# Optimization experiments

Measured on AMD Instinct MI355X. Metric: run time of the kernel, lower is better.

The kernel has to match this reference:

```python
import jax, jax.numpy as jnp
import numpy as np

B, T, E = 2, 2048, 2048
H, D = 16, 128
KVH = H // 2
THETA = 10000.0

def make_rope(dim, seq_len, theta):
    inv_freqs = 1.0 / (theta ** (jnp.arange(0, dim, 2, dtype=jnp.float32) / dim))
    positions = jnp.arange(seq_len, dtype=jnp.float32)
    freqs = positions[:, None] * inv_freqs[None, :]  # (T, D/2)
    return jax.lax.complex(jnp.cos(freqs), jnp.sin(freqs))

def apply_rope(x, rope):
    # x: (B, h, T, D), rope: (T, D/2) complex
    xr = x.astype(jnp.float32).reshape(*x.shape[:-1], -1, 2)
    xc = jax.lax.complex(xr[..., 0], xr[..., 1])
    out = xc * rope[None, None, :, :]
    return jnp.stack([jnp.real(out), jnp.imag(out)], axis=-1).reshape(x.shape).astype(x.dtype)

def setup_inputs() -> dict:
    key = jax.random.key(0)
    ks = jax.random.split(key, 5)
    x = jax.random.normal(ks[0], (B, T, E), dtype=jnp.float32)
    mask = jnp.tril(jnp.ones((T, T), dtype=jnp.int32))[None, None]  # causal (1,1,T,T)
    s = 0.02
    wq = jax.random.normal(ks[1], (E, H * D), dtype=jnp.float32) * s
    wk = jax.random.normal(ks[2], (E, KVH * D), dtype=jnp.float32) * s
    wv = jax.random.normal(ks[3], (E, KVH * D), dtype=jnp.float32) * s
    wo = jax.random.normal(ks[4], (H * D, E), dtype=jnp.float32) * s
    return {"x": x, "mask": mask, "wq": wq, "wk": wk, "wv": wv, "wo": wo}

def reference(x, mask, wq, wk, wv, wo):
    rope = make_rope(D, T, THETA)
    q = (x @ wq).reshape(B, T, H, D).transpose(0, 2, 1, 3)      # (B,H,T,D)
    k = (x @ wk).reshape(B, T, KVH, D).transpose(0, 2, 1, 3)    # (B,KVH,T,D)
    v = (x @ wv).reshape(B, T, KVH, D).transpose(0, 2, 1, 3)
    q = apply_rope(q, rope)
    k = apply_rope(k, rope)
    # GQA: repeat kv heads to match query heads
    k = jnp.repeat(k, H // KVH, axis=1)
    v = jnp.repeat(v, H // KVH, axis=1)
    scale = D ** -0.5
    attn = jnp.einsum('bhqd,bhkd->bhqk', q, k) * scale
    attn = jnp.where(mask == 0, -jnp.inf, attn)
    attn = jax.nn.softmax(attn, axis=-1)
    attn = jnp.where(jnp.isnan(attn), 0.0, attn)
    out = jnp.einsum('bhqk,bhkd->bhqd', attn, v)
    out = out.transpose(0, 2, 1, 3).reshape(B, T, H * D)
    return out @ wo
```

## Files before the change

### kernel.cpp

```cpp
#include <hip/hip_runtime.h>
#include <math.h>

#define Bb   2
#define Tt   2048
#define Ee   2048
#define Hh   16
#define KVHh 8
#define Dd   128
#define Mm   (Bb*Tt)

typedef unsigned short u16;
typedef __bf16 bf16x8 __attribute__((ext_vector_type(8)));
typedef float  f32x4  __attribute__((ext_vector_type(4)));

__device__ __forceinline__ u16 f2b(float f) {
    union { float f; unsigned u; } v; v.f = f;
    unsigned r = v.u + 0x7fffu + ((v.u >> 16) & 1u);
    return (u16)(r >> 16);
}
__device__ __forceinline__ u16 f2b_fast(float f) {
    union { float f; unsigned u; } v; v.f = f;
    return (u16)((v.u + 0x8000u) >> 16);
}
__device__ __forceinline__ float b2f(u16 h) {
    union { float f; unsigned u; } v; v.u = ((unsigned)h) << 16;
    return v.f;
}

__device__ __forceinline__ void gl_lds16(const u16* g, u16* l) {
    __builtin_amdgcn_global_load_lds(
        (const __attribute__((address_space(1))) void*)g,
        (__attribute__((address_space(3))) void*)l,
        16, 0, 0);
}

__global__ void cast_x_kernel(const float* __restrict__ x, u16* __restrict__ xb, int n4) {
    int i = blockIdx.x * blockDim.x + threadIdx.x;
    if (i >= n4) return;
    float4 f = ((const float4*)x)[i];
    unsigned lo = (unsigned)f2b(f.x) | ((unsigned)f2b(f.y) << 16);
    unsigned hi = (unsigned)f2b(f.z) | ((unsigned)f2b(f.w) << 16);
    ((uint2*)xb)[i] = make_uint2(lo, hi);
}

__global__ void transpose_cast4_kernel(const float* __restrict__ wq, const float* __restrict__ wk,
                                       const float* __restrict__ wv, const float* __restrict__ wo,
                                       u16* __restrict__ btqkv, u16* __restrict__ bto) {
    __shared__ float tile[32][33];
    int job = blockIdx.z;
    const float* W; u16* Bt; int C;
    if (job == 0)      { W = wq; Bt = btqkv;                      C = 2048; }
    else if (job == 1) { W = wk; Bt = btqkv + (size_t)2048 * Ee;  C = 1024; }
    else if (job == 2) { W = wv; Bt = btqkv + (size_t)3072 * Ee;  C = 1024; }
    else               { W = wo; Bt = bto;                        C = 2048; }
    int c0 = blockIdx.x * 32, r0 = blockIdx.y * 32;
    if (c0 >= C) return;
    int x = threadIdx.x, y = threadIdx.y;
    for (int j = y; j < 32; j += 8)
        tile[j][x] = W[(size_t)(r0 + j) * C + c0 + x];
    __syncthreads();
    for (int j = y; j < 32; j += 8)
        Bt[(size_t)(c0 + j) * 2048 + r0 + x] = f2b(tile[x][j]);
}

__global__ void transpose_v_kernel(const u16* __restrict__ v, u16* __restrict__ vt) {
    __shared__ u16 tile[32][34];
    int x = threadIdx.x, y = threadIdx.y;
    int c0 = blockIdx.x * 32;
    int r0 = blockIdx.y * 32;
    int bk = blockIdx.z;
    for (int j = y; j < 32; j += 8)
        tile[j][x] = v[((size_t)bk * Tt + r0 + j) * Dd + c0 + x];
    __syncthreads();
    for (int j = y; j < 32; j += 8)
        vt[((size_t)bk * Dd + c0 + j) * Tt + r0 + x] = tile[x][j];
}

__global__ void rope_kernel(u16* __restrict__ q, u16* __restrict__ k) {
    const int QP = Bb * Hh * Tt * (Dd / 2);
    const int KP = Bb * KVHh * Tt * (Dd / 2);
    int idx = blockIdx.x * blockDim.x + threadIdx.x;
    if (idx >= QP + KP) return;
    u16* ptr; int p;
    if (idx < QP) { ptr = q; p = idx; } else { ptr = k; p = idx - QP; }
    int d2 = p & 63;
    int row = p >> 6;
    int t = row & (Tt - 1);
    float ex = (float)(2 * d2) * (1.0f / 128.0f);
    float inv = expf(-ex * 9.210340371976184f);
    float fr = (float)t * inv;
    float c = cosf(fr), s = sinf(fr);
    size_t e0 = (size_t)row * Dd + 2 * d2;
    unsigned pair = *(const unsigned*)(ptr + e0);
    float x0 = b2f((u16)(pair & 0xffff));
    float x1 = b2f((u16)(pair >> 16));
    float o0 = x0 * c - x1 * s;
    float o1 = x0 * s + x1 * c;
    *(unsigned*)(ptr + e0) = (unsigned)f2b(o0) | ((unsigned)f2b(o1) << 16);
}

__global__ __launch_bounds__(256) void gemm_kernel(
    const u16* __restrict__ A, const u16* __restrict__ Bt,
    int Mdim, int Ndim, int Kdim, int mode,
    u16* __restrict__ qo, u16* __restrict__ ko, u16* __restrict__ vo,
    float* __restrict__ fo)
{
    __shared__ u16 Ash[128 * 64];
    __shared__ u16 Bsh[128 * 64];
    int tid = threadIdx.x;
    int lane = tid & 63, wv = tid >> 6;
    int quad = lane >> 4, l15 = lane & 15;
    int bn = blockIdx.x, bm = blockIdx.y;
    int wm = (wv >> 1) * 64, wn = (wv & 1) * 64;
    const int rowA0 = bm * 128, rowB0 = bn * 128;
    int srow = lane >> 3;
    int scol = (lane & 7) * 8;

    f32x4 acc[4][4];
#pragma unroll
    for (int i = 0; i < 4; i++)
#pragma unroll
        for (int j = 0; j < 4; j++) acc[i][j] = (f32x4){0.f, 0.f, 0.f, 0.f};

    for (int kb = 0; kb < Kdim; kb += 64) {
#pragma unroll
        for (int j = 0; j < 4; j++) {
            int chunk = wv * 4 + j;
            int r = chunk * 8 + srow;
            gl_lds16(A  + (size_t)(rowA0 + r) * Kdim + kb + scol, Ash + chunk * 512);
            gl_lds16(Bt + (size_t)(rowB0 + r) * Kdim + kb + scol, Bsh + chunk * 512);
        }
        __syncthreads();
#pragma unroll
        for (int kc = 0; kc < 2; kc++) {
            bf16x8 af[4], bfr[4];
#pragma unroll
            for (int i = 0; i < 4; i++)
                af[i] = *(const bf16x8*)(Ash + (wm + i * 16 + l15) * 64 + kc * 32 + quad * 8);
#pragma unroll
            for (int i = 0; i < 4; i++)
                bfr[i] = *(const bf16x8*)(Bsh + (wn + i * 16 + l15) * 64 + kc * 32 + quad * 8);
#pragma unroll
            for (int i = 0; i < 4; i++)
#pragma unroll
                for (int j = 0; j < 4; j++)
                    acc[i][j] = __builtin_amdgcn_mfma_f32_16x16x32_bf16(af[i], bfr[j], acc[i][j], 0, 0, 0);
        }
        __syncthreads();
    }

#pragma unroll
    for (int i = 0; i < 4; i++)
#pragma unroll
        for (int j = 0; j < 4; j++)
#pragma unroll
            for (int r = 0; r < 4; r++) {
                int m = rowA0 + wm + i * 16 + quad * 4 + r;
                int n = rowB0 + wn + j * 16 + l15;
                float val = acc[i][j][r];
                if (mode == 0) {
                    int b = m >> 11, t = m & (Tt - 1);
                    if (n < 2048) {
                        int h = n >> 7, d = n & 127;
                        qo[(((size_t)(b * Hh + h)) * Tt + t) * Dd + d] = f2b(val);
                    } else if (n < 3072) {
                        int h = (n - 2048) >> 7, d = n & 127;
                        ko[(((size_t)(b * KVHh + h)) * Tt + t) * Dd + d] = f2b(val);
                    } else {
                        int h = (n - 3072) >> 7, d = n & 127;
                        vo[(((size_t)(b * KVHh + h)) * Tt + t) * Dd + d] = f2b(val);
                    }
                } else {
                    fo[(size_t)m * Ndim + n] = val;
                }
            }
}

#define LDKV 136
#define LDVT 72
#define LDP  72

__global__ __launch_bounds__(256) void flash_kernel(
    const u16* __restrict__ q, const u16* __restrict__ k, const u16* __restrict__ vt,
    u16* __restrict__ attn)
{
    __shared__ u16 Ksh[64 * LDKV];
    __shared__ u16 Vtsh[128 * LDVT];
    __shared__ u16 Psh[128 * LDP];

    int tid = threadIdx.x, lane = tid & 63, w = tid >> 6;
    int quad = lane >> 4, l15 = lane & 15;
    int pr = blockIdx.x;
    int bh = blockIdx.y;
    int b = bh >> 4, h = bh & 15;
    int kvh = h >> 1;
    const u16* qbase = q + (size_t)bh * Tt * Dd;
    const u16* kbase = k + ((size_t)(b * KVHh + kvh)) * Tt * Dd;
    const u16* vtbase = vt + ((size_t)(b * KVHh + kvh)) * Dd * Tt;
    u16* P0 = Psh + (2 * w) * 16 * LDP;
    u16* P1 = Psh + (2 * w + 1) * 16 * LDP;
    const float sc2 = 0.08838834764831845f * 1.4426950408889634f;

    for (int half = 0; half < 2; half++) {
        int qt = half ? (15 - pr) : pr;
        int row0 = qt * 128 + w * 32;

        bf16x8 qf0[4], qf1[4];
        {
            const u16* qr0 = qbase + (size_t)(row0 + l15) * Dd + quad * 8;
            const u16* qr1 = qbase + (size_t)(row0 + 16 + l15) * Dd + quad * 8;
#pragma unroll
            for (int c = 0; c < 4; c++) {
                qf0[c] = *(const bf16x8*)(qr0 + c * 32);
                qf1[c] = *(const bf16x8*)(qr1 + c * 32);
            }
        }

        f32x4 o0[8], o1[8];
#pragma unroll
        for (int i = 0; i < 8; i++) { o0[i] = (f32x4){0.f,0.f,0.f,0.f}; o1[i] = (f32x4){0.f,0.f,0.f,0.f}; }
        float l0[4] = {0.f,0.f,0.f,0.f}, l1[4] = {0.f,0.f,0.f,0.f};

        int nkt = 2 * (qt + 1);
        for (int kt = 0; kt < nkt; kt++) {
#pragma unroll
            for (int j = 0; j < 4; j++) {
                int chunk = j * 256 + tid;
                int rk = chunk >> 4, ck = chunk & 15;
                uint4 dk = *(const uint4*)(kbase + (size_t)(kt * 64 + rk) * Dd + ck * 8);
                *(uint4*)(Ksh + rk * LDKV + ck * 8) = dk;
                int rv = chunk >> 3, cv = chunk & 7;
                uint4 dv = *(const uint4*)(vtbase + (size_t)rv * Tt + kt * 64 + cv * 8);
                *(uint4*)(Vtsh + rv * LDVT + cv * 8) = dv;
            }
            __syncthreads();

            bool skip = (kt * 64) > (row0 + 31);
            if (!skip) {
                f32x4 s0[4], s1[4];
#pragma unroll
                for (int ni = 0; ni < 4; ni++) { s0[ni] = (f32x4){0.f,0.f,0.f,0.f}; s1[ni] = (f32x4){0.f,0.f,0.f,0.f}; }
#pragma unroll
                for (int c = 0; c < 4; c++)
#pragma unroll
                    for (int ni = 0; ni < 4; ni++) {
                        bf16x8 kf = *(const bf16x8*)(Ksh + (ni * 16 + l15) * LDKV + c * 32 + quad * 8);
                        s0[ni] = __builtin_amdgcn_mfma_f32_16x16x32_bf16(qf0[c], kf, s0[ni], 0, 0, 0);
                        s1[ni] = __builtin_amdgcn_mfma_f32_16x16x32_bf16(qf1[c], kf, s1[ni], 0, 0, 0);
                    }

                if (kt * 64 + 63 > row0) {
#pragma unroll
                    for (int ni = 0; ni < 4; ni++)
#pragma unroll
                        for (int r = 0; r < 4; r++) {
                            int kcol = kt * 64 + ni * 16 + l15;
                            int qa = row0 + quad * 4 + r;
                            int qb2 = row0 + 16 + quad * 4 + r;
                            if (kcol > qa)  s0[ni][r] = -__builtin_inff();
                            if (kcol > qb2) s1[ni][r] = -__builtin_inff();
                        }
                }

#pragma unroll
                for (int ni = 0; ni < 4; ni++)
#pragma unroll
                    for (int r = 0; r < 4; r++) {
                        float p0 = exp2f(s0[ni][r] * sc2);
                        l0[r] += p0;
                        P0[(quad * 4 + r) * LDP + ni * 16 + l15] = f2b_fast(p0);
                        float p1 = exp2f(s1[ni][r] * sc2);
                        l1[r] += p1;
                        P1[(quad * 4 + r) * LDP + ni * 16 + l15] = f2b_fast(p1);
                    }
            }
            __syncthreads();

            if (!skip) {
#pragma unroll
                for (int c = 0; c < 2; c++) {
                    bf16x8 pf0 = *(const bf16x8*)(P0 + l15 * LDP + c * 32 + quad * 8);
                    bf16x8 pf1 = *(const bf16x8*)(P1 + l15 * LDP + c * 32 + quad * 8);
#pragma unroll
                    for (int di = 0; di < 8; di++) {
                        bf16x8 vf = *(const bf16x8*)(Vtsh + (di * 16 + l15) * LDVT + c * 32 + quad * 8);
                        o0[di] = __builtin_amdgcn_mfma_f32_16x16x32_bf16(pf0, vf, o0[di], 0, 0, 0);
                        o1[di] = __builtin_amdgcn_mfma_f32_16x16x32_bf16(pf1, vf, o1[di], 0, 0, 0);
                    }
                }
            }
            __syncthreads();
        }

        float linv0[4], linv1[4];
#pragma unroll
        for (int r = 0; r < 4; r++) {
            float a = l0[r];
            a += __shfl_xor(a, 1); a += __shfl_xor(a, 2);
            a += __shfl_xor(a, 4); a += __shfl_xor(a, 8);
            linv0[r] = 1.0f / a;
            float c2 = l1[r];
            c2 += __shfl_xor(c2, 1); c2 += __shfl_xor(c2, 2);
            c2 += __shfl_xor(c2, 4); c2 += __shfl_xor(c2, 8);
            linv1[r] = 1.0f / c2;
        }
#pragma unroll
        for (int di = 0; di < 8; di++)
#pragma unroll
            for (int r = 0; r < 4; r++) {
                int ta = row0 + quad * 4 + r;
                int tb = row0 + 16 + quad * 4 + r;
                size_t ma = (size_t)b * Tt + ta;
                size_t mb = (size_t)b * Tt + tb;
                attn[ma * (Hh * Dd) + h * Dd + di * 16 + l15] = f2b(o0[di][r] * linv0[r]);
                attn[mb * (Hh * Dd) + h * Dd + di * 16 + l15] = f2b(o1[di][r] * linv1[r]);
            }
        __syncthreads();
    }
}

extern "C" void kernel_launch(void* const* d_in, const int* in_sizes, int n_in,
                              void* d_out, int out_size, void* d_ws, size_t ws_size,
                              hipStream_t stream) {
    const float* x  = (const float*)d_in[0];
    const float* wq = (const float*)d_in[2];
    const float* wk = (const float*)d_in[3];
    const float* wv = (const float*)d_in[4];
    const float* wo = (const float*)d_in[5];
    float* out = (float*)d_out;

    char* ws = (char*)d_ws;
    u16* xb    = (u16*)ws; ws += (size_t)Mm * Ee * 2;
    u16* btqkv = (u16*)ws; ws += (size_t)4096 * Ee * 2;
    u16* bto   = (u16*)ws; ws += (size_t)Ee * (Hh * Dd) * 2;
    u16* qb    = (u16*)ws; ws += (size_t)Bb * Hh * Tt * Dd * 2;
    u16* kb    = (u16*)ws; ws += (size_t)Bb * KVHh * Tt * Dd * 2;
    u16* vb    = (u16*)ws; ws += (size_t)Bb * KVHh * Tt * Dd * 2;
    u16* vtb   = (u16*)ws; ws += (size_t)Bb * KVHh * Dd * Tt * 2;
    u16* attn  = (u16*)ws; ws += (size_t)Mm * (Hh * Dd) * 2;

    cast_x_kernel<<<(Mm * Ee / 4 + 255) / 256, 256, 0, stream>>>(x, xb, Mm * Ee / 4);

    transpose_cast4_kernel<<<dim3(64, 64, 4), dim3(32, 8), 0, stream>>>(wq, wk, wv, wo, btqkv, bto);

    gemm_kernel<<<dim3(32, 32), 256, 0, stream>>>(xb, btqkv, Mm, 4096, Ee, 0,
                                                  qb, kb, vb, nullptr);

    {
        int total = Bb * Hh * Tt * 64 + Bb * KVHh * Tt * 64;
        rope_kernel<<<(total + 255) / 256, 256, 0, stream>>>(qb, kb);
    }

    transpose_v_kernel<<<dim3(Dd / 32, Tt / 32, Bb * KVHh), dim3(32, 8), 0, stream>>>(vb, vtb);

    flash_kernel<<<dim3(Tt / 256, Bb * Hh), 256, 0, stream>>>(qb, kb, vtb, attn);

    gemm_kernel<<<dim3(16, 32), 256, 0, stream>>>(attn, bto, Mm, 2048, Hh * Dd, 1,
                                                  nullptr, nullptr, nullptr, out);
}
```

Baseline: 406.8 us.

## Replace GEMM with 256x256-tile, 8-wave, double-buffered pipelined kernel

Swaps the 128x128 single-buffered GEMM for a 256x256 tile kernel with 8 waves, double-buffered LDS, and XOR-swizzled columns. Global-to-LDS loads for the next K tile are interleaved with four MFMA phases per iteration, using explicit vmcnt waits, barriers and setprio. The aim is to hide load latency, avoid LDS bank conflicts and raise arithmetic intensity for both the QKV and output projections. In exchange it uses 128KB of LDS per block and launches far fewer blocks: 256 for the QKV projection and 128 for the output projection, which may underfill the GPU's compute units.

```diff
diff --git a/kernel.cpp b/kernel.cpp
--- a/kernel.cpp
+++ b/kernel.cpp
@@ -99,58 +99,167 @@
     *(unsigned*)(ptr + e0) = (unsigned)f2b(o0) | ((unsigned)f2b(o1) << 16);
 }
 
-__global__ __launch_bounds__(256) void gemm_kernel(
+__global__ __launch_bounds__(512, 2) void gemm8_kernel(
     const u16* __restrict__ A, const u16* __restrict__ Bt,
-    int Mdim, int Ndim, int Kdim, int mode,
+    int Ndim, int Kdim, int mode,
     u16* __restrict__ qo, u16* __restrict__ ko, u16* __restrict__ vo,
     float* __restrict__ fo)
 {
-    __shared__ u16 Ash[128 * 64];
-    __shared__ u16 Bsh[128 * 64];
-    int tid = threadIdx.x;
-    int lane = tid & 63, wv = tid >> 6;
-    int quad = lane >> 4, l15 = lane & 15;
-    int bn = blockIdx.x, bm = blockIdx.y;
-    int wm = (wv >> 1) * 64, wn = (wv & 1) * 64;
-    const int rowA0 = bm * 128, rowB0 = bn * 128;
-    int srow = lane >> 3;
-    int scol = (lane & 7) * 8;
-
-    f32x4 acc[4][4];
-#pragma unroll
-    for (int i = 0; i < 4; i++)
+    __shared__ u16 sm[2][2][256 * 64];
+    const int tid = threadIdx.x;
+    const int lane = tid & 63, w = tid >> 6;
+    const int quad = lane >> 4, l15 = lane & 15;
+    const int hl = (l15 >> 2) & 3;
+    const int bn = blockIdx.x, bm = blockIdx.y;
+    const int wm = (w >> 2) * 128, wn = (w & 3) * 64;
+    const int rowA0 = bm * 256, rowB0 = bn * 256;
+
+    const int srow = lane >> 3;
+    const int sj4  = ((lane >> 5) & 1) << 4;
+    const int scol = (lane & 7) * 8;
+    const int wa = w & 3, wb = w >> 2;
+    const int cAlo = (wm >> 3) + 2 * wa;
+    const int cAhi = (wm >> 3) + 8 + 2 * wa;
+    const int cBlo = (wn >> 3) + 2 * wb;
+    const int cBhi = (wn >> 3) + 4 + 2 * wb;
+
+    const int col0 = (quad * 8) ^ (hl << 4);
+    const int col1 = (32 + quad * 8) ^ (hl << 4);
+
+    f32x4 acc[8][4];
+#pragma unroll
+    for (int i = 0; i < 8; i++)
 #pragma unroll
         for (int j = 0; j < 4; j++) acc[i][j] = (f32x4){0.f, 0.f, 0.f, 0.f};
 
-    for (int kb = 0; kb < Kdim; kb += 64) {
-#pragma unroll
-        for (int j = 0; j < 4; j++) {
-            int chunk = wv * 4 + j;
-            int r = chunk * 8 + srow;
-            gl_lds16(A  + (size_t)(rowA0 + r) * Kdim + kb + scol, Ash + chunk * 512);
-            gl_lds16(Bt + (size_t)(rowB0 + r) * Kdim + kb + scol, Bsh + chunk * 512);
-        }
-        __syncthreads();
-#pragma unroll
-        for (int kc = 0; kc < 2; kc++) {
-            bf16x8 af[4], bfr[4];
+#define STAGE_PAIR(G, Grow0, ldsb, cb, kk) do { \
+    gl_lds16((G) + (size_t)((Grow0) + (cb) * 8 + srow) * Kdim + (kk) + (scol ^ sj4), \
+             (ldsb) + (cb) * 512); \
+    gl_lds16((G) + (size_t)((Grow0) + (cb) * 8 + 8 + srow) * Kdim + (kk) + (scol ^ sj4 ^ 32), \
+             (ldsb) + (cb) * 512 + 512); \
+} while (0)
+
+    STAGE_PAIR(A,  rowA0, &sm[0][0][0], cAlo, 0);
+    STAGE_PAIR(Bt, rowB0, &sm[0][1][0], cBlo, 0);
+    STAGE_PAIR(Bt, rowB0, &sm[0][1][0], cBhi, 0);
+    STAGE_PAIR(A,  rowA0, &sm[0][0][0], cAhi, 0);
+    asm volatile("s_waitcnt vmcnt(4)" ::: "memory");
+    __builtin_amdgcn_s_barrier();
+    __builtin_amdgcn_sched_barrier(0);
+
+    bf16x8 a4[4][2], bA[2][2], bB[2][2];
+    const int NT = Kdim >> 6;
+
+    for (int t = 0; t < NT; ++t) {
+        u16* As = &sm[t & 1][0][0];
+        u16* Bs = &sm[t & 1][1][0];
+        u16* An = &sm[(t + 1) & 1][0][0];
+        u16* Bn = &sm[(t + 1) & 1][1][0];
+        const int kk = (t + 1) << 6;
+        const bool st = (t + 1 < NT);
+
+#pragma unroll
+        for (int i = 0; i < 4; i++) {
+            const u16* p = As + (wm + i * 16 + l15) * 64;
+            a4[i][0] = *(const bf16x8*)(p + col0);
+            a4[i][1] = *(const bf16x8*)(p + col1);
+        }
+#pragma unroll
+        for (int j = 0; j < 2; j++) {
+            const u16* p = Bs + (wn + j * 16 + l15) * 64;
+            bA[j][0] = *(const bf16x8*)(p + col0);
+            bA[j][1] = *(const bf16x8*)(p + col1);
+        }
+        if (st) STAGE_PAIR(A, rowA0, An, cAlo, kk);
+        __builtin_amdgcn_sched_barrier(0);
+        __builtin_amdgcn_s_barrier();
+        __builtin_amdgcn_sched_barrier(0);
+        __builtin_amdgcn_s_setprio(1);
+#pragma unroll
+        for (int kc = 0; kc < 2; kc++)
 #pragma unroll
             for (int i = 0; i < 4; i++)
-                af[i] = *(const bf16x8*)(Ash + (wm + i * 16 + l15) * 64 + kc * 32 + quad * 8);
+#pragma unroll
+                for (int j = 0; j < 2; j++)
+                    acc[i][j] = __builtin_amdgcn_mfma_f32_16x16x32_bf16(a4[i][kc], bA[j][kc], acc[i][j], 0, 0, 0);
+        __builtin_amdgcn_s_setprio(0);
+        __builtin_amdgcn_sched_barrier(0);
+        if (st) { asm volatile("s_waitcnt vmcnt(4)" ::: "memory"); }
+        else    { asm volatile("s_waitcnt vmcnt(2)" ::: "memory"); }
+        __builtin_amdgcn_s_barrier();
+        __builtin_amdgcn_sched_barrier(0);
+
+#pragma unroll
+        for (int j = 0; j < 2; j++) {
+            const u16* p = Bs + (wn + 32 + j * 16 + l15) * 64;
+            bB[j][0] = *(const bf16x8*)(p + col0);
+            bB[j][1] = *(const bf16x8*)(p + col1);
+        }
+        if (st) STAGE_PAIR(Bt, rowB0, Bn, cBlo, kk);
+        __builtin_amdgcn_sched_barrier(0);
+        __builtin_amdgcn_s_barrier();
+        __builtin_amdgcn_sched_barrier(0);
+        __builtin_amdgcn_s_setprio(1);
+#pragma unroll
+        for (int kc = 0; kc < 2; kc++)
 #pragma unroll
             for (int i = 0; i < 4; i++)
-                bfr[i] = *(const bf16x8*)(Bsh + (wn + i * 16 + l15) * 64 + kc * 32 + quad * 8);
+#pragma unroll
+                for (int j = 0; j < 2; j++)
+                    acc[i][j + 2] = __builtin_amdgcn_mfma_f32_16x16x32_bf16(a4[i][kc], bB[j][kc], acc[i][j + 2], 0, 0, 0);
+        __builtin_amdgcn_s_setprio(0);
+        __builtin_amdgcn_sched_barrier(0);
+        if (st) { asm volatile("s_waitcnt vmcnt(4)" ::: "memory"); }
+        else    { asm volatile("s_waitcnt vmcnt(0)" ::: "memory"); }
+        __builtin_amdgcn_s_barrier();
+        __builtin_amdgcn_sched_barrier(0);
+
+#pragma unroll
+        for (int i = 0; i < 4; i++) {
+            const u16* p = As + (wm + 64 + i * 16 + l15) * 64;
+            a4[i][0] = *(const bf16x8*)(p + col0);
+            a4[i][1] = *(const bf16x8*)(p + col1);
+        }
+        if (st) STAGE_PAIR(Bt, rowB0, Bn, cBhi, kk);
+        __builtin_amdgcn_sched_barrier(0);
+        __builtin_amdgcn_s_barrier();
+        __builtin_amdgcn_sched_barrier(0);
+        __builtin_amdgcn_s_setprio(1);
+#pragma unroll
+        for (int kc = 0; kc < 2; kc++)
 #pragma unroll
             for (int i = 0; i < 4; i++)
 #pragma unroll
-                for (int j = 0; j < 4; j++)
-                    acc[i][j] = __builtin_amdgcn_mfma_f32_16x16x32_bf16(af[i], bfr[j], acc[i][j], 0, 0, 0);
-        }
-        __syncthreads();
+                for (int j = 0; j < 2; j++)
+                    acc[i + 4][j] = __builtin_amdgcn_mfma_f32_16x16x32_bf16(a4[i][kc], bA[j][kc], acc[i + 4][j], 0, 0, 0);
+        __builtin_amdgcn_s_setprio(0);
+        __builtin_amdgcn_sched_barrier(0);
+        if (st) { asm volatile("s_waitcnt vmcnt(4)" ::: "memory"); }
+        __builtin_amdgcn_s_barrier();
+        __builtin_amdgcn_sched_barrier(0);
+
+        if (st) STAGE_PAIR(A, rowA0, An, cAhi, kk);
+        __builtin_amdgcn_sched_barrier(0);
+        __builtin_amdgcn_s_barrier();
+        __builtin_amdgcn_sched_barrier(0);
+        __builtin_amdgcn_s_setprio(1);
+#pragma unroll
+        for (int kc = 0; kc < 2; kc++)
+#pragma unroll
+            for (int i = 0; i < 4; i++)
+#pragma unroll
+                for (int j = 0; j < 2; j++)
+                    acc[i + 4][j + 2] = __builtin_amdgcn_mfma_f32_16x16x32_bf16(a4[i][kc], bB[j][kc], acc[i + 4][j + 2], 0, 0, 0);
+        __builtin_amdgcn_s_setprio(0);
+        __builtin_amdgcn_sched_barrier(0);
+        if (st) { asm volatile("s_waitcnt vmcnt(4)" ::: "memory"); }
+        __builtin_amdgcn_s_barrier();
+        __builtin_amdgcn_sched_barrier(0);
     }
-
-#pragma unroll
-    for (int i = 0; i < 4; i++)
+#undef STAGE_PAIR
+
+#pragma unroll
+    for (int i = 0; i < 8; i++)
 #pragma unroll
         for (int j = 0; j < 4; j++)
 #pragma unroll
@@ -159,16 +268,16 @@
                 int n = rowB0 + wn + j * 16 + l15;
                 float val = acc[i][j][r];
                 if (mode == 0) {
-                    int b = m >> 11, t = m & (Tt - 1);
+                    int b = m >> 11, tq = m & (Tt - 1);
                     if (n < 2048) {
                         int h = n >> 7, d = n & 127;
-                        qo[(((size_t)(b * Hh + h)) * Tt + t) * Dd + d] = f2b(val);
+                        qo[(((size_t)(b * Hh + h)) * Tt + tq) * Dd + d] = f2b(val);
                     } else if (n < 3072) {
                         int h = (n - 2048) >> 7, d = n & 127;
-                        ko[(((size_t)(b * KVHh + h)) * Tt + t) * Dd + d] = f2b(val);
+                        ko[(((size_t)(b * KVHh + h)) * Tt + tq) * Dd + d] = f2b(val);
                     } else {
                         int h = (n - 3072) >> 7, d = n & 127;
-                        vo[(((size_t)(b * KVHh + h)) * Tt + t) * Dd + d] = f2b(val);
+                        vo[(((size_t)(b * KVHh + h)) * Tt + tq) * Dd + d] = f2b(val);
                     }
                 } else {
                     fo[(size_t)m * Ndim + n] = val;
@@ -343,8 +452,8 @@
 
     transpose_cast4_kernel<<<dim3(64, 64, 4), dim3(32, 8), 0, stream>>>(wq, wk, wv, wo, btqkv, bto);
 
-    gemm_kernel<<<dim3(32, 32), 256, 0, stream>>>(xb, btqkv, Mm, 4096, Ee, 0,
-                                                  qb, kb, vb, nullptr);
+    gemm8_kernel<<<dim3(16, 16), 512, 0, stream>>>(xb, btqkv, 4096, Ee, 0,
+                                                   qb, kb, vb, nullptr);
 
     {
         int total = Bb * Hh * Tt * 64 + Bb * KVHh * Tt * 64;
@@ -355,6 +464,6 @@
 
     flash_kernel<<<dim3(Tt / 256, Bb * Hh), 256, 0, stream>>>(qb, kb, vtb, attn);
 
-    gemm_kernel<<<dim3(16, 32), 256, 0, stream>>>(attn, bto, Mm, 2048, Hh * Dd, 1,
+    gemm8_kernel<<<dim3(8, 16), 512, 0, stream>>>(attn, bto, 2048, Hh * Dd, 1,
                                                   nullptr, nullptr, nullptr, out);
 }
```

New measurement: 399.6 us. About the same (-1.8%).
